# Optimization experiments

Hardware: AMD Instinct MI355X
Metric: run time of the kernel (lower is better)

The kernel has to match this reference:

```python
import jax, jax.numpy as jnp
import numpy as np

N = 50000        # nodes
E = 300000       # edges (before self-loops)
F_IN = 128       # input feature dim
H = 2            # attention heads
D = 128          # per-head dim (hidden_dim/heads)
C = 3            # output classes
G = 64           # graphs in batch
NEG_SLOPE = 0.2  # PyG GATConv default leaky-relu slope


def setup_inputs() -> dict:
    key = jax.random.key(0)
    ks = jax.random.split(key, 9)
    x = jax.random.normal(ks[0], (N, F_IN), jnp.float32)
    edge_index = jax.random.randint(ks[1], (2, E), 0, N, dtype=jnp.int64)
    batch = jnp.sort(jax.random.randint(ks[2], (N,), 0, G, dtype=jnp.int64))
    W = jax.random.normal(ks[3], (F_IN, H, D), jnp.float32) * 0.05   # GAT lin weight
    att_src = jax.random.normal(ks[4], (H, D), jnp.float32) * 0.1
    att_dst = jax.random.normal(ks[5], (H, D), jnp.float32) * 0.1
    bias_gat = jax.random.normal(ks[6], (H * D,), jnp.float32) * 0.01
    fc_w = jax.random.normal(ks[7], (H * D, C), jnp.float32) * 0.05
    fc_b = jax.random.normal(ks[8], (C,), jnp.float32) * 0.01
    a = jnp.array(1.0, jnp.float32)
    return dict(x=x, edge_index=edge_index, batch=batch, W=W, att_src=att_src,
                att_dst=att_dst, bias_gat=bias_gat, fc_w=fc_w, fc_b=fc_b, a=a)


def reference(x, edge_index, batch, W, att_src, att_dst, bias_gat, fc_w, fc_b, a):
    n = x.shape[0]
    # PyG GATConv adds self-loops by default
    loops = jnp.arange(n, dtype=edge_index.dtype)
    src = jnp.concatenate([edge_index[0], loops])   # message sources j
    tgt = jnp.concatenate([edge_index[1], loops])   # message targets i

    xw = jnp.einsum('nf,nfhd->nhd', x[:, :, None, None] * 0 + x[:, :, None, None], W[None]) if False else jnp.einsum('nf,fhd->nhd', x, W)  # [N,H,D]
    a_s = jnp.sum(xw * att_src, axis=-1)            # [N,H]
    a_d = jnp.sum(xw * att_dst, axis=-1)            # [N,H]

    e = a_s[src] + a_d[tgt]                         # [E+N,H]
    e = jnp.where(e > 0, e, NEG_SLOPE * e)          # leaky relu
    # segment softmax over incoming edges of each target node
    m = jax.ops.segment_max(e, tgt, num_segments=n)
    ex = jnp.exp(e - m[tgt])
    denom = jax.ops.segment_sum(ex, tgt, num_segments=n)
    alpha = ex / denom[tgt]                         # [E+N,H]

    out = jax.ops.segment_sum(alpha[:, :, None] * xw[src], tgt, num_segments=n)  # [N,H,D]
    z = out.reshape(n, H * D) + bias_gat
    z = jax.nn.relu(z)
    z = z @ fc_w + fc_b                              # [N,C]
    z = jax.nn.log_softmax(z, axis=1)
    z = jax.ops.segment_sum(z, batch, num_segments=G)  # global_add_pool -> [G,C]
    z = a * z
    return jax.nn.log_softmax(z, axis=1)
```

## Files before the change

kernel.cpp:

```cpp
#include <hip/hip_runtime.h>
#include <hip/hip_bf16.h>

typedef __hip_bfloat16 bf16;
typedef __attribute__((ext_vector_type(8))) short bf16x8;
typedef __attribute__((ext_vector_type(4))) float f32x4;

#define F_IN    128
#define HD      256
#define N_C     3
#define N_G     64
#define NEG_SLOPE 0.2f
#define NPART   512
#define DMAX    32

__device__ __forceinline__ float b2f(unsigned short u) {
    return __uint_as_float(((unsigned int)u) << 16);
}
__device__ __forceinline__ unsigned short f2bs(float f) {
    unsigned int u = __float_as_uint(f);
    return (unsigned short)((u + 0x7FFFu + ((u >> 16) & 1u)) >> 16);
}

__global__ void scatter_kernel(const int* __restrict__ ei, int* __restrict__ cnt,
                               int* __restrict__ ssrc32,
                               const float* __restrict__ W,
                               unsigned short* __restrict__ WTf, int e) {
    int i = blockIdx.x * blockDim.x + threadIdx.x;
    if (i < HD * F_IN) {
        int j = i & 7;
        int L = (i >> 3) & 63;
        int c = (i >> 9) & 3;
        int t = i >> 11;
        int f  = c * 32 + (L >> 4) * 8 + j;
        int hd = t * 16 + (L & 15);
        WTf[i] = f2bs(W[f * HD + hd]);
    }
    int i2 = i * 2;
    if (i2 < e) {
        int2 s2 = *(const int2*)(ei + i2);
        int2 t2 = *(const int2*)(ei + e + i2);
        int p = atomicAdd(&cnt[t2.x], 1);
        if (p < DMAX) ssrc32[(size_t)t2.x * DMAX + p] = s2.x;
        if (i2 + 1 < e) {
            p = atomicAdd(&cnt[t2.y], 1);
            if (p < DMAX) ssrc32[(size_t)t2.y * DMAX + p] = s2.y;
        }
    }
}

__global__ __launch_bounds__(256) void xw_mfma_kernel(const float* __restrict__ x,
                                                      const uint4* __restrict__ WTf,
                                                      bf16* __restrict__ xw,
                                                      const float* __restrict__ att_src,
                                                      const float* __restrict__ att_dst,
                                                      float* __restrict__ asd, int n) {
    __shared__ uint4 wt_lds[4096];
    int tid = threadIdx.x;
    int wid = tid >> 6, lane = tid & 63;
    int r16 = lane & 15, quad = lane >> 4;
    int rb = blockIdx.x * 64 + wid * 16;
    bool valid = rb < n;
    int rbl = valid ? rb : 0;

    const float* xr = x + (size_t)(rbl + r16) * F_IN + quad * 8;
    float4 f0a = *(const float4*)(xr + 0);
    float4 f1a = *(const float4*)(xr + 4);
    float4 f0b = *(const float4*)(xr + 32);
    float4 f1b = *(const float4*)(xr + 36);
    float4 f0c = *(const float4*)(xr + 64);
    float4 f1c = *(const float4*)(xr + 68);
    float4 f0d = *(const float4*)(xr + 96);
    float4 f1d = *(const float4*)(xr + 100);

    #pragma unroll
    for (int r = 0; r < 16; r++)
        wt_lds[r * 256 + tid] = WTf[r * 256 + tid];

    bf16x8 xf[4];
    {
        bf16x8 a;
        a[0]=(short)f2bs(f0a.x); a[1]=(short)f2bs(f0a.y); a[2]=(short)f2bs(f0a.z); a[3]=(short)f2bs(f0a.w);
        a[4]=(short)f2bs(f1a.x); a[5]=(short)f2bs(f1a.y); a[6]=(short)f2bs(f1a.z); a[7]=(short)f2bs(f1a.w);
        xf[0]=a;
        a[0]=(short)f2bs(f0b.x); a[1]=(short)f2bs(f0b.y); a[2]=(short)f2bs(f0b.z); a[3]=(short)f2bs(f0b.w);
        a[4]=(short)f2bs(f1b.x); a[5]=(short)f2bs(f1b.y); a[6]=(short)f2bs(f1b.z); a[7]=(short)f2bs(f1b.w);
        xf[1]=a;
        a[0]=(short)f2bs(f0c.x); a[1]=(short)f2bs(f0c.y); a[2]=(short)f2bs(f0c.z); a[3]=(short)f2bs(f0c.w);
        a[4]=(short)f2bs(f1c.x); a[5]=(short)f2bs(f1c.y); a[6]=(short)f2bs(f1c.z); a[7]=(short)f2bs(f1c.w);
        xf[2]=a;
        a[0]=(short)f2bs(f0d.x); a[1]=(short)f2bs(f0d.y); a[2]=(short)f2bs(f0d.z); a[3]=(short)f2bs(f0d.w);
        a[4]=(short)f2bs(f1d.x); a[5]=(short)f2bs(f1d.y); a[6]=(short)f2bs(f1d.z); a[7]=(short)f2bs(f1d.w);
        xf[3]=a;
    }
    __syncthreads();

    const unsigned short* wls = (const unsigned short*)wt_lds;
    float s0a = 0.f, s1a = 0.f, d0a = 0.f, d1a = 0.f;
    for (int t = 0; t < 16; t++) {
        f32x4 acc = {0.f, 0.f, 0.f, 0.f};
        #pragma unroll
        for (int c = 0; c < 4; c++) {
            bf16x8 wf = *(const bf16x8*)(wls + ((t * 4 + c) * 64 + lane) * 8);
            acc = __builtin_amdgcn_mfma_f32_16x16x32_bf16(wf, xf[c], acc, 0, 0, 0);
        }
        int colbase = t * 16;
        float4 as4 = *(const float4*)(att_src + colbase + quad * 4);
        float4 ad4 = *(const float4*)(att_dst + colbase + quad * 4);
        if (valid) {
            unsigned int w0 = (unsigned int)f2bs(acc[0]) | ((unsigned int)f2bs(acc[1]) << 16);
            unsigned int w1 = (unsigned int)f2bs(acc[2]) | ((unsigned int)f2bs(acc[3]) << 16);
            *(uint2*)((unsigned short*)xw + (size_t)(rb + r16) * HD + colbase + quad * 4)
                = make_uint2(w0, w1);
        }
        float ds = acc[0]*as4.x + acc[1]*as4.y + acc[2]*as4.z + acc[3]*as4.w;
        float dd = acc[0]*ad4.x + acc[1]*ad4.y + acc[2]*ad4.z + acc[3]*ad4.w;
        if (t < 8) { s0a += ds; d0a += dd; }
        else       { s1a += ds; d1a += dd; }
    }

    #pragma unroll
    for (int o = 16; o <= 32; o <<= 1) {
        s0a += __shfl_xor(s0a, o, 64);
        s1a += __shfl_xor(s1a, o, 64);
        d0a += __shfl_xor(d0a, o, 64);
        d1a += __shfl_xor(d1a, o, 64);
    }
    if (valid && quad == 0) {
        float4 v;
        v.x = s0a; v.y = s1a; v.z = d0a; v.w = d1a;
        ((float4*)asd)[rb + r16] = v;
    }
}

__global__ __launch_bounds__(256) void main_kernel(const bf16* __restrict__ xw,
                                                   const float* __restrict__ asd,
                                                   const int* __restrict__ cnt,
                                                   const int* __restrict__ ssrc32,
                                                   const int* __restrict__ batch,
                                                   const float* __restrict__ bias,
                                                   const float* __restrict__ fcw,
                                                   const float* __restrict__ fcb,
                                                   float* __restrict__ gsumP, int n) {
    __shared__ int   sidx[4][64];
    __shared__ float salp[4][2][64];
    int wid = threadIdx.x >> 6, lane = threadIdx.x & 63;
    int head = lane >> 5;
    int node = blockIdx.x * 4 + wid;
    if (node >= n) return;

    float4 my = ((const float4*)asd)[node];
    float ad0 = my.z, ad1 = my.w;
    int dege = cnt[node];
    if (dege > DMAX) dege = DMAX;
    int deg = dege + 1;
    const int* srow = ssrc32 + (size_t)node * DMAX;

    float a0 = 0.f, a1 = 0.f, a2 = 0.f, a3 = 0.f;

    bool act = lane < deg;
    int myidx = node;
    float e0 = -1e30f, e1 = -1e30f;
    if (lane < dege) {
        myidx = srow[lane];
        float4 sa = ((const float4*)asd)[myidx];
        e0 = sa.x + ad0;
        e1 = sa.y + ad1;
    } else if (lane == dege) {
        e0 = my.x + ad0;
        e1 = my.y + ad1;
    }
    e0 = (e0 > 0.f) ? e0 : NEG_SLOPE * e0;
    e1 = (e1 > 0.f) ? e1 : NEG_SLOPE * e1;
    if (!act) { e0 = -1e30f; e1 = -1e30f; }

    float m0 = e0, m1 = e1;
    #pragma unroll
    for (int o = 1; o <= 8; o <<= 1) {
        m0 = fmaxf(m0, __shfl_xor(m0, o, 64));
        m1 = fmaxf(m1, __shfl_xor(m1, o, 64));
    }
    if (deg > 16) {
        #pragma unroll
        for (int o = 16; o <= 32; o <<= 1) {
            m0 = fmaxf(m0, __shfl_xor(m0, o, 64));
            m1 = fmaxf(m1, __shfl_xor(m1, o, 64));
        }
    }
    float al0 = act ? __expf(e0 - m0) : 0.f;
    float al1 = act ? __expf(e1 - m1) : 0.f;
    float s0 = al0, s1 = al1;
    #pragma unroll
    for (int o = 1; o <= 8; o <<= 1) {
        s0 += __shfl_xor(s0, o, 64);
        s1 += __shfl_xor(s1, o, 64);
    }
    if (deg > 16) {
        #pragma unroll
        for (int o = 16; o <= 32; o <<= 1) {
            s0 += __shfl_xor(s0, o, 64);
            s1 += __shfl_xor(s1, o, 64);
        }
    }
    sidx[wid][lane] = myidx;
    salp[wid][0][lane] = act ? al0 / s0 : 0.f;
    salp[wid][1][lane] = act ? al1 / s1 : 0.f;

    int nb = (deg + 7) >> 3;
    for (int b = 0; b < nb; b++) {
        int eb = b * 8;
        int idx[8]; ushort4 v[8]; float w[8];
        #pragma unroll
        for (int k = 0; k < 8; k++) idx[k] = sidx[wid][eb + k];
        #pragma unroll
        for (int k = 0; k < 8; k++)
            v[k] = ((const ushort4*)(xw + (size_t)idx[k] * HD))[lane];
        #pragma unroll
        for (int k = 0; k < 8; k++) w[k] = salp[wid][head][eb + k];
        #pragma unroll
        for (int k = 0; k < 8; k++) {
            a0 += w[k] * b2f(v[k].x); a1 += w[k] * b2f(v[k].y);
            a2 += w[k] * b2f(v[k].z); a3 += w[k] * b2f(v[k].w);
        }
    }

    float4 bv = ((const float4*)bias)[lane];
    float z0 = fmaxf(a0 + bv.x, 0.f);
    float z1 = fmaxf(a1 + bv.y, 0.f);
    float z2 = fmaxf(a2 + bv.z, 0.f);
    float z3 = fmaxf(a3 + bv.w, 0.f);

    const float* fp = fcw + lane * 12;
    float4 c0 = *(const float4*)(fp);
    float4 c1 = *(const float4*)(fp + 4);
    float4 c2 = *(const float4*)(fp + 8);
    float l0 = z0 * c0.x + z1 * c0.w + z2 * c1.z + z3 * c2.y;
    float l1 = z0 * c0.y + z1 * c1.x + z2 * c1.w + z3 * c2.z;
    float l2 = z0 * c0.z + z1 * c1.y + z2 * c2.x + z3 * c2.w;
    #pragma unroll
    for (int o = 32; o > 0; o >>= 1) {
        l0 += __shfl_xor(l0, o, 64);
        l1 += __shfl_xor(l1, o, 64);
        l2 += __shfl_xor(l2, o, 64);
    }
    if (lane == 0) {
        l0 += fcb[0]; l1 += fcb[1]; l2 += fcb[2];
        float m = fmaxf(l0, fmaxf(l1, l2));
        float lse = m + __logf(__expf(l0 - m) + __expf(l1 - m) + __expf(l2 - m));
        int b = batch[node];
        int part = node & (NPART - 1);
        atomicAdd(&gsumP[(b * 3 + 0) * NPART + part], l0 - lse);
        atomicAdd(&gsumP[(b * 3 + 1) * NPART + part], l1 - lse);
        atomicAdd(&gsumP[(b * 3 + 2) * NPART + part], l2 - lse);
    }
}

__global__ __launch_bounds__(64) void final_kernel(const float* __restrict__ gsumP,
                                                   const float* __restrict__ a,
                                                   float* __restrict__ out) {
    int g = blockIdx.x;
    int lane = threadIdx.x;
    float v[3];
    #pragma unroll
    for (int c = 0; c < 3; c++) {
        float s = 0.f;
        for (int p = lane; p < NPART; p += 64)
            s += gsumP[(g * 3 + c) * NPART + p];
        #pragma unroll
        for (int o = 32; o > 0; o >>= 1) s += __shfl_xor(s, o, 64);
        v[c] = s;
    }
    if (lane == 0) {
        float av = a[0];
        float v0 = v[0] * av, v1 = v[1] * av, v2 = v[2] * av;
        float m = fmaxf(v0, fmaxf(v1, v2));
        float lse = m + __logf(__expf(v0 - m) + __expf(v1 - m) + __expf(v2 - m));
        out[g * 3 + 0] = v0 - lse;
        out[g * 3 + 1] = v1 - lse;
        out[g * 3 + 2] = v2 - lse;
    }
}

extern "C" void kernel_launch(void* const* d_in, const int* in_sizes, int n_in,
                              void* d_out, int out_size, void* d_ws, size_t ws_size,
                              hipStream_t stream) {
    const float* x       = (const float*)d_in[0];
    const int*   ei      = (const int*)d_in[1];
    const int*   batch   = (const int*)d_in[2];
    const float* W       = (const float*)d_in[3];
    const float* att_src = (const float*)d_in[4];
    const float* att_dst = (const float*)d_in[5];
    const float* bias    = (const float*)d_in[6];
    const float* fcw     = (const float*)d_in[7];
    const float* fcb     = (const float*)d_in[8];
    const float* a_scale = (const float*)d_in[9];
    float* out = (float*)d_out;

    const int n = in_sizes[2];
    const int e = in_sizes[1] / 2;

    char* ws = (char*)d_ws;
    bf16*  xw     = (bf16*)ws;
    float* asd    = (float*)(ws + 25600000);
    int*   cnt    = (int*)(ws + 26400000);
    float* gsumP  = (float*)(ws + 26600000);
    int*   ssrc32 = (int*)(ws + 26993280);
    unsigned short* WTf = (unsigned short*)(ws + 33393280);

    hipMemsetAsync(cnt, 0, (size_t)n * 4 + (size_t)N_G * N_C * NPART * 4, stream);

    int eb256 = (e / 2 + 255) / 256;
    hipLaunchKernelGGL(scatter_kernel, dim3(eb256), dim3(256), 0, stream,
                       ei, cnt, ssrc32, W, WTf, e);
    hipLaunchKernelGGL(xw_mfma_kernel, dim3((n + 63) / 64), dim3(256), 0, stream,
                       x, (const uint4*)WTf, xw, att_src, att_dst, asd, n);
    hipLaunchKernelGGL(main_kernel,    dim3((n + 3) / 4), dim3(256), 0, stream,
                       xw, asd, cnt, ssrc32, batch, bias, fcw, fcb, gsumP, n);
    hipLaunchKernelGGL(final_kernel,   dim3(N_G), dim3(64), 0, stream, gsumP, a_scale, out);
}
```

Before: 165.8 us.

## Process two nodes per wavefront with 16-byte bf16 gathers per lane

The aggregation kernel now gives each node a half-wavefront (32 lanes) instead of a full wave, so each wave handles two nodes. Each lane gathers 8 bf16 features with one 16-byte load, and edges are processed in groups of 4. Softmax and FC reductions shrink to 32-lane shuffles, and the grid is halved. The aim is to cut idle lanes and per-node overhead for low-degree nodes and to issue wider memory transactions. In exchange, the degree cap drops to 31, and the padded edge loop can read shared memory slightly past a node's row when the degree is high.

After: 159.1 us. -4.0%, faster.

```diff
diff --git a/kernel.cpp b/kernel.cpp
--- a/kernel.cpp
+++ b/kernel.cpp
@@ -144,105 +144,113 @@
     __shared__ int   sidx[4][64];
     __shared__ float salp[4][2][64];
     int wid = threadIdx.x >> 6, lane = threadIdx.x & 63;
-    int head = lane >> 5;
-    int node = blockIdx.x * 4 + wid;
+    int half = lane >> 5;
+    int ll   = lane & 31;
+    int hsel = (ll >> 4) & 1;
+    int node = blockIdx.x * 8 + wid * 2 + half;
     if (node >= n) return;
 
     float4 my = ((const float4*)asd)[node];
     float ad0 = my.z, ad1 = my.w;
     int dege = cnt[node];
-    if (dege > DMAX) dege = DMAX;
+    if (dege > 31) dege = 31;
     int deg = dege + 1;
     const int* srow = ssrc32 + (size_t)node * DMAX;
 
-    float a0 = 0.f, a1 = 0.f, a2 = 0.f, a3 = 0.f;
-
-    bool act = lane < deg;
     int myidx = node;
     float e0 = -1e30f, e1 = -1e30f;
-    if (lane < dege) {
-        myidx = srow[lane];
+    if (ll < dege) {
+        myidx = srow[ll];
         float4 sa = ((const float4*)asd)[myidx];
         e0 = sa.x + ad0;
         e1 = sa.y + ad1;
-    } else if (lane == dege) {
+    } else if (ll == dege) {
         e0 = my.x + ad0;
         e1 = my.y + ad1;
     }
     e0 = (e0 > 0.f) ? e0 : NEG_SLOPE * e0;
     e1 = (e1 > 0.f) ? e1 : NEG_SLOPE * e1;
+    bool act = ll < deg;
     if (!act) { e0 = -1e30f; e1 = -1e30f; }
 
     float m0 = e0, m1 = e1;
     #pragma unroll
-    for (int o = 1; o <= 8; o <<= 1) {
+    for (int o = 1; o <= 16; o <<= 1) {
         m0 = fmaxf(m0, __shfl_xor(m0, o, 64));
         m1 = fmaxf(m1, __shfl_xor(m1, o, 64));
-    }
-    if (deg > 16) {
-        #pragma unroll
-        for (int o = 16; o <= 32; o <<= 1) {
-            m0 = fmaxf(m0, __shfl_xor(m0, o, 64));
-            m1 = fmaxf(m1, __shfl_xor(m1, o, 64));
-        }
     }
     float al0 = act ? __expf(e0 - m0) : 0.f;
     float al1 = act ? __expf(e1 - m1) : 0.f;
     float s0 = al0, s1 = al1;
     #pragma unroll
-    for (int o = 1; o <= 8; o <<= 1) {
+    for (int o = 1; o <= 16; o <<= 1) {
         s0 += __shfl_xor(s0, o, 64);
         s1 += __shfl_xor(s1, o, 64);
-    }
-    if (deg > 16) {
-        #pragma unroll
-        for (int o = 16; o <= 32; o <<= 1) {
-            s0 += __shfl_xor(s0, o, 64);
-            s1 += __shfl_xor(s1, o, 64);
-        }
     }
     sidx[wid][lane] = myidx;
     salp[wid][0][lane] = act ? al0 / s0 : 0.f;
     salp[wid][1][lane] = act ? al1 / s1 : 0.f;
 
-    int nb = (deg + 7) >> 3;
-    for (int b = 0; b < nb; b++) {
-        int eb = b * 8;
-        int idx[8]; ushort4 v[8]; float w[8];
-        #pragma unroll
-        for (int k = 0; k < 8; k++) idx[k] = sidx[wid][eb + k];
-        #pragma unroll
-        for (int k = 0; k < 8; k++)
-            v[k] = ((const ushort4*)(xw + (size_t)idx[k] * HD))[lane];
-        #pragma unroll
-        for (int k = 0; k < 8; k++) w[k] = salp[wid][head][eb + k];
-        #pragma unroll
-        for (int k = 0; k < 8; k++) {
-            a0 += w[k] * b2f(v[k].x); a1 += w[k] * b2f(v[k].y);
-            a2 += w[k] * b2f(v[k].z); a3 += w[k] * b2f(v[k].w);
-        }
-    }
-
-    float4 bv = ((const float4*)bias)[lane];
-    float z0 = fmaxf(a0 + bv.x, 0.f);
-    float z1 = fmaxf(a1 + bv.y, 0.f);
-    float z2 = fmaxf(a2 + bv.z, 0.f);
-    float z3 = fmaxf(a3 + bv.w, 0.f);
-
-    const float* fp = fcw + lane * 12;
+    int degmax = max(deg, __shfl_xor(deg, 32, 64));
+    int base = half << 5;
+    const unsigned short* xwp = (const unsigned short*)xw + (size_t)ll * 8;
+    float a[8] = {0,0,0,0,0,0,0,0};
+    for (int b = 0; b < degmax; b += 4) {
+        int i0 = sidx[wid][base + b + 0];
+        int i1 = sidx[wid][base + b + 1];
+        int i2 = sidx[wid][base + b + 2];
+        int i3 = sidx[wid][base + b + 3];
+        uint4 u0 = *(const uint4*)(xwp + (size_t)i0 * HD);
+        uint4 u1 = *(const uint4*)(xwp + (size_t)i1 * HD);
+        uint4 u2 = *(const uint4*)(xwp + (size_t)i2 * HD);
+        uint4 u3 = *(const uint4*)(xwp + (size_t)i3 * HD);
+        float w0 = salp[wid][hsel][base + b + 0];
+        float w1 = salp[wid][hsel][base + b + 1];
+        float w2 = salp[wid][hsel][base + b + 2];
+        float w3 = salp[wid][hsel][base + b + 3];
+        a[0] += w0 * __uint_as_float(u0.x << 16) + w1 * __uint_as_float(u1.x << 16)
+              + w2 * __uint_as_float(u2.x << 16) + w3 * __uint_as_float(u3.x << 16);
+        a[1] += w0 * __uint_as_float(u0.x & 0xFFFF0000u) + w1 * __uint_as_float(u1.x & 0xFFFF0000u)
+              + w2 * __uint_as_float(u2.x & 0xFFFF0000u) + w3 * __uint_as_float(u3.x & 0xFFFF0000u);
+        a[2] += w0 * __uint_as_float(u0.y << 16) + w1 * __uint_as_float(u1.y << 16)
+              + w2 * __uint_as_float(u2.y << 16) + w3 * __uint_as_float(u3.y << 16);
+        a[3] += w0 * __uint_as_float(u0.y & 0xFFFF0000u) + w1 * __uint_as_float(u1.y & 0xFFFF0000u)
+              + w2 * __uint_as_float(u2.y & 0xFFFF0000u) + w3 * __uint_as_float(u3.y & 0xFFFF0000u);
+        a[4] += w0 * __uint_as_float(u0.z << 16) + w1 * __uint_as_float(u1.z << 16)
+              + w2 * __uint_as_float(u2.z << 16) + w3 * __uint_as_float(u3.z << 16);
+        a[5] += w0 * __uint_as_float(u0.z & 0xFFFF0000u) + w1 * __uint_as_float(u1.z & 0xFFFF0000u)
+              + w2 * __uint_as_float(u2.z & 0xFFFF0000u) + w3 * __uint_as_float(u3.z & 0xFFFF0000u);
+        a[6] += w0 * __uint_as_float(u0.w << 16) + w1 * __uint_as_float(u1.w << 16)
+              + w2 * __uint_as_float(u2.w << 16) + w3 * __uint_as_float(u3.w << 16);
+        a[7] += w0 * __uint_as_float(u0.w & 0xFFFF0000u) + w1 * __uint_as_float(u1.w & 0xFFFF0000u)
+              + w2 * __uint_as_float(u2.w & 0xFFFF0000u) + w3 * __uint_as_float(u3.w & 0xFFFF0000u);
+    }
+
+    const float* bp = bias + ll * 8;
+    float4 b0 = *(const float4*)(bp);
+    float4 b1 = *(const float4*)(bp + 4);
+    float z0 = fmaxf(a[0] + b0.x, 0.f), z1 = fmaxf(a[1] + b0.y, 0.f);
+    float z2 = fmaxf(a[2] + b0.z, 0.f), z3 = fmaxf(a[3] + b0.w, 0.f);
+    float z4 = fmaxf(a[4] + b1.x, 0.f), z5 = fmaxf(a[5] + b1.y, 0.f);
+    float z6 = fmaxf(a[6] + b1.z, 0.f), z7 = fmaxf(a[7] + b1.w, 0.f);
+
+    const float* fp = fcw + ll * 24;
     float4 c0 = *(const float4*)(fp);
     float4 c1 = *(const float4*)(fp + 4);
     float4 c2 = *(const float4*)(fp + 8);
-    float l0 = z0 * c0.x + z1 * c0.w + z2 * c1.z + z3 * c2.y;
-    float l1 = z0 * c0.y + z1 * c1.x + z2 * c1.w + z3 * c2.z;
-    float l2 = z0 * c0.z + z1 * c1.y + z2 * c2.x + z3 * c2.w;
-    #pragma unroll
-    for (int o = 32; o > 0; o >>= 1) {
+    float4 c3 = *(const float4*)(fp + 12);
+    float4 c4 = *(const float4*)(fp + 16);
+    float4 c5 = *(const float4*)(fp + 20);
+    float l0 = z0*c0.x + z1*c0.w + z2*c1.z + z3*c2.y + z4*c3.x + z5*c3.w + z6*c4.z + z7*c5.y;
+    float l1 = z0*c0.y + z1*c1.x + z2*c1.w + z3*c2.z + z4*c3.y + z5*c4.x + z6*c4.w + z7*c5.z;
+    float l2 = z0*c0.z + z1*c1.y + z2*c2.x + z3*c2.w + z4*c3.z + z5*c4.y + z6*c5.x + z7*c5.w;
+    #pragma unroll
+    for (int o = 1; o <= 16; o <<= 1) {
         l0 += __shfl_xor(l0, o, 64);
         l1 += __shfl_xor(l1, o, 64);
         l2 += __shfl_xor(l2, o, 64);
     }
-    if (lane == 0) {
+    if (ll == 0) {
         l0 += fcb[0]; l1 += fcb[1]; l2 += fcb[2];
         float m = fmaxf(l0, fmaxf(l1, l2));
         float lse = m + __logf(__expf(l0 - m) + __expf(l1 - m) + __expf(l2 - m));
@@ -313,7 +321,7 @@
                        ei, cnt, ssrc32, W, WTf, e);
     hipLaunchKernelGGL(xw_mfma_kernel, dim3((n + 63) / 64), dim3(256), 0, stream,
                        x, (const uint4*)WTf, xw, att_src, att_dst, asd, n);
-    hipLaunchKernelGGL(main_kernel,    dim3((n + 3) / 4), dim3(256), 0, stream,
+    hipLaunchKernelGGL(main_kernel,    dim3((n + 7) / 8), dim3(256), 0, stream,
                        xw, asd, cnt, ssrc32, batch, bias, fcw, fcb, gsumP, n);
     hipLaunchKernelGGL(final_kernel,   dim3(N_G), dim3(64), 0, stream, gsumP, a_scale, out);
 }
```
